# Performance work log

Measured on AMD Instinct MI355X. Metric: run time of the kernel, lower is better.

Reference implementation:

```python
import jax, jax.numpy as jnp
import numpy as np

PERIODS = [4, 2, 1]   # base_periods[:n_period]
TEMPERATURE = 0.1
TOPM = 20
EPS = 1e-12


def _l2norm(v, axis):
    n = jnp.sqrt(jnp.sum(v * v, axis=axis, keepdims=True))
    return v / jnp.maximum(n, EPS)


def decompose_mg(x):
    """x: [B, L, C] -> mg: [G, B, L, C] (offset removed, as in torch code)."""
    B, L, C = x.shape
    mg = []
    for g in PERIODS:
        cur = x.reshape(B, L // g, g, C).mean(axis=2)      # unfold(size=g, step=g).mean(-1)
        cur = jnp.repeat(cur, g, axis=1)                   # repeat_interleave back to L
        mg.append(cur)
    mg = jnp.stack(mg, axis=0)                             # [G, B, L, C]
    return mg - mg[:, :, -1:, :]                           # remove per-series last-step offset


def extract_channel_state(mg):
    """mg: [G, B, L, C] -> [G, B, C, 4] (mean, std, slope, mean |diff|)."""
    L = mg.shape[2]
    mean = mg.mean(axis=2)
    std = mg.std(axis=2)                                   # unbiased=False (ddof=0)
    slope = (mg[:, :, -1, :] - mg[:, :, 0, :]) / float(L - 1)
    abs_diff = jnp.abs(mg[:, :, 1:, :] - mg[:, :, :-1, :]).mean(axis=2)
    return jnp.stack([mean, std, slope, abs_diff], axis=-1)


def setup_inputs() -> dict:
    key = jax.random.key(0)
    k1, k2, k3 = jax.random.split(key, 3)
    B, L, C, G, T, P = 32, 512, 64, 3, 10000, 96
    x = jax.random.normal(k1, (B, L, C), dtype=jnp.float32)
    pool_state = jax.random.normal(k2, (G, T, C, 4), dtype=jnp.float32)
    y_pool = jax.random.normal(k3, (T, P, C), dtype=jnp.float32)
    return {"x": x, "pool_state": pool_state, "y_pool": y_pool}


def reference(x, pool_state, y_pool):
    # Multi-scale decomposition of query batch
    q_mg = decompose_mg(x)                                  # [G, B, L, C]
    q_state = extract_channel_state(q_mg)                   # [G, B, C, 4]
    # Normalized channel-state similarity vs candidate pool
    q = _l2norm(q_state, axis=-1)
    p = _l2norm(pool_state, axis=-1)
    sim = jnp.einsum('gbcd,gtcd->gbct', q, p)               # [G, B, C, T]
    sim = sim.mean(axis=0)                                  # combine granularities -> [B, C, T]
    # Top-m retrieval per (batch, channel)
    vals, idx = jax.lax.top_k(sim, TOPM)                    # [B, C, M]
    w = jax.nn.softmax(vals / TEMPERATURE, axis=-1)         # [B, C, M]
    # Gather retrieved future windows, channelwise: y_pool [T, P, C]
    C = y_pool.shape[2]
    y_ct = jnp.transpose(y_pool, (2, 0, 1))                 # [C, T, P]
    gathered = y_ct[jnp.arange(C)[None, :, None], idx]      # [B, C, M, P]
    out = jnp.einsum('bcm,bcmp->bpc', w, gathered)          # [B, P, C]
    return out
```

## Files before the change

kernel.cpp:

```cpp
#include <hip/hip_runtime.h>
#include <hip/hip_fp16.h>
#include <math.h>

#define NB 32
#define NL 512
#define NC 64
#define NG 3
#define NT 10000
#define NP 96
#define TOPM 20
#define M1 8
#define NCH 256
#define CHUNK 40
#define QK 16
#define NCAND 64
#define PNBLK 1250
#define P16STR ((size_t)NT * NC)

union H2U { uint2 u; __half2 h[2]; };

__global__ __launch_bounds__(512) void pre_kernel(const float* __restrict__ x,
                                                  const float* __restrict__ ps,
                                                  double* __restrict__ q,
                                                  uint2* __restrict__ phat16) {
  __shared__ double s_sum[8][3][64], s_sq[8][3][64], s_abs[8][3][64];
  __shared__ double s_first[3][64], s_last[3][64];
  if (blockIdx.x < NB) {
    const int b = blockIdx.x, w = threadIdx.x >> 6, c = threadIdx.x & 63;
    const float* xp = x + (size_t)b * NL * NC + c;
    const int l0 = w * 64;
    double sum[3] = {0, 0, 0}, sumsq[3] = {0, 0, 0}, sumabs[3] = {0, 0, 0};
    double prev[3] = {0, 0, 0}, first[3] = {0, 0, 0};
    if (w > 0) {
      double e0 = xp[(l0 - 4) * NC], e1 = xp[(l0 - 3) * NC];
      double e2 = xp[(l0 - 2) * NC], e3 = xp[(l0 - 1) * NC];
      prev[2] = e3; prev[1] = (e2 + e3) * 0.5; prev[0] = (e0 + e1 + e2 + e3) * 0.25;
    }
    double acc2 = 0.0, acc4 = 0.0;
    for (int i = 0; i < 64; ++i) {
      const int l = l0 + i;
      double v = (double)xp[l * NC];
      sum[2] += v; sumsq[2] += v * v;
      if (l == 0) first[2] = v; else sumabs[2] += fabs(v - prev[2]);
      prev[2] = v;
      acc2 += v;
      if (l & 1) {
        double cur = acc2 * 0.5; acc2 = 0.0;
        sum[1] += cur; sumsq[1] += cur * cur;
        if (l == 1) first[1] = cur; else sumabs[1] += fabs(cur - prev[1]);
        prev[1] = cur;
      }
      acc4 += v;
      if ((l & 3) == 3) {
        double cur = acc4 * 0.25; acc4 = 0.0;
        sum[0] += cur; sumsq[0] += cur * cur;
        if (l == 3) first[0] = cur; else sumabs[0] += fabs(cur - prev[0]);
        prev[0] = cur;
      }
    }
    for (int g = 0; g < 3; ++g) {
      s_sum[w][g][c] = sum[g]; s_sq[w][g][c] = sumsq[g]; s_abs[w][g][c] = sumabs[g];
    }
    if (w == 0) { for (int g = 0; g < 3; ++g) s_first[g][c] = first[g]; }
    if (w == 7) { for (int g = 0; g < 3; ++g) s_last[g][c] = prev[g]; }
    __syncthreads();
    if (w == 0) {
      const double J[3] = {128.0, 256.0, 512.0};
      for (int g = 0; g < 3; ++g) {
        double S = 0, Q2 = 0, A = 0;
        for (int ww = 0; ww < 8; ++ww) {
          S += s_sum[ww][g][c]; Q2 += s_sq[ww][g][c]; A += s_abs[ww][g][c];
        }
        double mean = S / J[g];
        double var = Q2 / J[g] - mean * mean; if (var < 0.0) var = 0.0;
        double last = s_last[g][c];
        double s0 = mean - last;
        double s1 = sqrt(var);
        double s2 = (last - s_first[g][c]) * (1.0 / 511.0);
        double s3 = A * (1.0 / 511.0);
        double n = sqrt(s0 * s0 + s1 * s1 + s2 * s2 + s3 * s3);
        double inv = 1.0 / fmax(n, 1e-12);
        double* qp = q + ((((size_t)g * NB) + b) * NC + c) * 4;
        qp[0] = s0 * inv; qp[1] = s1 * inv; qp[2] = s2 * inv; qp[3] = s3 * inv;
      }
    }
  } else {
    const int i = (blockIdx.x - NB) * 512 + threadIdx.x;
    if (i < NT * NC) {
#pragma unroll
      for (int g = 0; g < 3; ++g) {
        const size_t off = ((size_t)g * NT * NC + i) * 4;
        const float4 pv = *reinterpret_cast<const float4*>(ps + off);
        double p0 = pv.x, p1 = pv.y, p2 = pv.z, p3 = pv.w;
        double inv = 1.0 / fmax(sqrt(p0 * p0 + p1 * p1 + p2 * p2 + p3 * p3), 1e-12);
        H2U o;
        o.h[0] = __halves2half2(__float2half_rn((float)(p0 * inv)),
                                __float2half_rn((float)(p1 * inv)));
        o.h[1] = __halves2half2(__float2half_rn((float)(p2 * inv)),
                                __float2half_rn((float)(p3 * inv)));
        phat16[(size_t)g * P16STR + i] = o.u;
      }
    }
  }
}

__device__ __forceinline__ void insert8(float s, int ti, float val[M1], int idx[M1]) {
  float cv = s; int ci = ti;
#pragma unroll
  for (int m = 0; m < M1; ++m) {
    bool sw = cv > val[m];
    float tv = sw ? val[m] : cv; int tx = sw ? idx[m] : ci;
    val[m] = sw ? cv : val[m];   idx[m] = sw ? ci : idx[m];
    cv = tv; ci = tx;
  }
}

#if defined(__has_builtin)
#if __has_builtin(__builtin_amdgcn_fdot2)
#define HAVE_FDOT2 1
#endif
#endif

__device__ __forceinline__ float sim_dot(const uint2* __restrict__ p16,
                                         size_t o,
#ifdef HAVE_FDOT2
                                         const __half2 qh[6]
#else
                                         const float qv[12]
#endif
                                         ) {
  H2U a0, a1, a2;
  a0.u = p16[o];
  a1.u = p16[P16STR + o];
  a2.u = p16[2 * P16STR + o];
#ifdef HAVE_FDOT2
  float s = 0.f;
  s = __builtin_amdgcn_fdot2(qh[0], a0.h[0], s, false);
  s = __builtin_amdgcn_fdot2(qh[1], a0.h[1], s, false);
  s = __builtin_amdgcn_fdot2(qh[2], a1.h[0], s, false);
  s = __builtin_amdgcn_fdot2(qh[3], a1.h[1], s, false);
  s = __builtin_amdgcn_fdot2(qh[4], a2.h[0], s, false);
  s = __builtin_amdgcn_fdot2(qh[5], a2.h[1], s, false);
  return s;
#else
  float2 f0 = __half22float2(a0.h[0]), f1 = __half22float2(a0.h[1]);
  float2 f2 = __half22float2(a1.h[0]), f3 = __half22float2(a1.h[1]);
  float2 f4 = __half22float2(a2.h[0]), f5 = __half22float2(a2.h[1]);
  return qv[0] * f0.x + qv[1] * f0.y + qv[2] * f1.x + qv[3] * f1.y +
         qv[4] * f2.x + qv[5] * f2.y + qv[6] * f3.x + qv[7] * f3.y +
         qv[8] * f4.x + qv[9] * f4.y + qv[10] * f5.x + qv[11] * f5.y;
#endif
}

__global__ __launch_bounds__(1024, 8) void sim32_kernel(
    const uint2* __restrict__ p16, const double* __restrict__ q,
    float* __restrict__ cval, int* __restrict__ cidx) {
  const int wav = threadIdx.x >> 6;
  const int c = threadIdx.x & 63;
  const int b = blockIdx.x * 16 + wav;
  const int ch = blockIdx.y;
#ifdef HAVE_FDOT2
  __half2 qh[6];
#pragma unroll
  for (int g = 0; g < 3; ++g) {
    const double* qp = q + ((((size_t)g * NB) + b) * NC + c) * 4;
    qh[g * 2 + 0] = __halves2half2(__float2half_rn((float)(qp[0] * (1.0 / 3.0))),
                                   __float2half_rn((float)(qp[1] * (1.0 / 3.0))));
    qh[g * 2 + 1] = __halves2half2(__float2half_rn((float)(qp[2] * (1.0 / 3.0))),
                                   __float2half_rn((float)(qp[3] * (1.0 / 3.0))));
  }
#else
  float qv[12];
#pragma unroll
  for (int g = 0; g < 3; ++g) {
    const double* qp = q + ((((size_t)g * NB) + b) * NC + c) * 4;
#pragma unroll
    for (int j = 0; j < 4; ++j) qv[g * 4 + j] = (float)(qp[j] * (1.0 / 3.0));
  }
#endif
  float val[M1]; int idx[M1];
#pragma unroll
  for (int m = 0; m < M1; ++m) { val[m] = -1e30f; idx[m] = 0; }
  int t0 = ch * CHUNK;
  int t1 = t0 + CHUNK; if (t1 > NT) t1 = NT;
  for (int t = t0; t + 1 < t1; t += 2) {
    const size_t oA = (size_t)t * NC + c;
    const size_t oB = oA + NC;
#ifdef HAVE_FDOT2
    float sA = sim_dot(p16, oA, qh);
    float sB = sim_dot(p16, oB, qh);
#else
    float sA = sim_dot(p16, oA, qv);
    float sB = sim_dot(p16, oB, qv);
#endif
    if (sA > val[M1 - 1]) insert8(sA, t, val, idx);
    if (sB > val[M1 - 1]) insert8(sB, t + 1, val, idx);
  }
  float* vo = cval + ((((size_t)b * NC) + c) * NCH + ch) * M1;
  int* io = cidx + ((((size_t)b * NC) + c) * NCH + ch) * M1;
#pragma unroll
  for (int m = 0; m < M1; ++m) { vo[m] = val[m]; io[m] = idx[m]; }
}

__device__ __forceinline__ unsigned long long mk_key(float v, int t) {
  unsigned u = __float_as_uint(v);
  u = (u & 0x80000000u) ? ~u : (u | 0x80000000u);
  return ((unsigned long long)u << 32) | (unsigned long long)(0xFFFFFFFFu - (unsigned)t);
}

__global__ __launch_bounds__(128) void merge_gather_kernel(
    const float* __restrict__ cval, const int* __restrict__ cidx,
    const float* __restrict__ ps, const double* __restrict__ q,
    const float* __restrict__ y, float* __restrict__ out) {
  const int c = blockIdx.x, b = blockIdx.y;
  __shared__ float v_s[NCH * M1];
  __shared__ int i_s[NCH * M1];
  __shared__ int ct_s[NCAND];
  __shared__ double rv_s[NCAND];
  __shared__ double m0_s, inv_s;
  __shared__ double e_s[TOPM];
  __shared__ int ts_s[TOPM];
  __shared__ float w2_s[TOPM];
  __shared__ int t2_s[TOPM];
  const int n = NCH * M1;
  const size_t row = (size_t)b * NC + c;
  const float4* vin = reinterpret_cast<const float4*>(cval + row * n);
  const int4* iin = reinterpret_cast<const int4*>(cidx + row * n);
  for (int k = threadIdx.x; k < n / 4; k += 128) {
    *reinterpret_cast<float4*>(&v_s[k * 4]) = vin[k];
    *reinterpret_cast<int4*>(&i_s[k * 4]) = iin[k];
  }
  __syncthreads();
  {
    const int w = threadIdx.x >> 6, lane = threadIdx.x & 63;
    const int lane32 = lane & 31;
    const int qtr = (w << 1) | (lane >> 5);
    const int l0 = (qtr * 64 + lane32 * 2) * M1;
    const int l1 = l0 + M1;
    int p0 = 0, p1 = 0;
    unsigned long long k0 = mk_key(v_s[l0], i_s[l0]);
    unsigned long long k1 = mk_key(v_s[l1], i_s[l1]);
    for (int r = 0; r < QK; ++r) {
      unsigned long long me = k0 > k1 ? k0 : k1;
      unsigned long long km = me;
#pragma unroll
      for (int st = 1; st < 32; st <<= 1) {
        unsigned long long k2 = __shfl_xor(km, st);
        km = k2 > km ? k2 : km;
      }
      if (lane32 == r)
        ct_s[qtr * QK + r] = (int)(0xFFFFFFFFu - (unsigned)(km & 0xFFFFFFFFull));
      if (me == km) {
        if (k0 >= k1) {
          ++p0; k0 = (p0 < M1) ? mk_key(v_s[l0 + p0], i_s[l0 + p0]) : 0ull;
        } else {
          ++p1; k1 = (p1 < M1) ? mk_key(v_s[l1 + p1], i_s[l1 + p1]) : 0ull;
        }
      }
    }
  }
  __syncthreads();
  double myv = -1e300; int myt = 0x7fffffff;
  if (threadIdx.x < NCAND) {
    myt = ct_s[threadIdx.x];
    double s = 0.0;
#pragma unroll
    for (int g = 0; g < 3; ++g) {
      const double* qp = q + ((((size_t)g * NB) + b) * NC + c) * 4;
      const float4 pv = *reinterpret_cast<const float4*>(
          ps + ((((size_t)g * NT) + myt) * NC + c) * 4);
      double pp0 = pv.x, pp1 = pv.y, pp2 = pv.z, pp3 = pv.w;
      double ss = pp0 * pp0 + pp1 * pp1 + pp2 * pp2 + pp3 * pp3;
      double dot = qp[0] * pp0 + qp[1] * pp1 + qp[2] * pp2 + qp[3] * pp3;
      s += dot / fmax(sqrt(ss), 1e-12);
    }
    myv = s * (1.0 / 3.0);
    rv_s[threadIdx.x] = myv;
  }
  __syncthreads();
  int rank = -1;
  if (threadIdx.x < NCAND) {
    rank = 0;
    for (int j = 0; j < NCAND; ++j) {
      double vj = rv_s[j]; int tj = ct_s[j];
      rank += (vj > myv) || (vj == myv && tj < myt);
    }
    if (rank == 0) m0_s = myv;
  }
  __syncthreads();
  if (rank >= 0 && rank < TOPM) { e_s[rank] = exp((myv - m0_s) * 10.0); ts_s[rank] = myt; }
  __syncthreads();
  if (threadIdx.x == 0) {
    double sum = 0.0;
#pragma unroll
    for (int m = 0; m < TOPM; ++m) sum += e_s[m];
    inv_s = 1.0 / sum;
  }
  __syncthreads();
  if (threadIdx.x < TOPM) {
    const int t = ts_s[threadIdx.x];
    int pos = 0;
#pragma unroll
    for (int j = 0; j < TOPM; ++j) pos += (ts_s[j] < t);
    w2_s[pos] = (float)(e_s[threadIdx.x] * inv_s);
    t2_s[pos] = t;
  }
  __syncthreads();
  const int p = threadIdx.x;
  if (p < NP) {
    float acc = 0.f;
#pragma unroll
    for (int m = 0; m < TOPM; ++m)
      acc += w2_s[m] * y[(((size_t)t2_s[m]) * NP + p) * NC + c];
    out[(((size_t)b * NP) + p) * NC + c] = acc;
  }
}

__global__ __launch_bounds__(256) void sim_topk_inline_kernel(
    const float* __restrict__ ps, const double* __restrict__ q,
    double* __restrict__ cval, int* __restrict__ cidx, int nch, int chunk) {
  const int wav = threadIdx.x >> 6;
  const int c = threadIdx.x & 63;
  const int b = blockIdx.y * 4 + wav;
  const int ch = blockIdx.x;
  double qv[3][4];
#pragma unroll
  for (int g = 0; g < 3; ++g) {
    const double* qp = q + ((((size_t)g * NB) + b) * NC + c) * 4;
    qv[g][0] = qp[0]; qv[g][1] = qp[1]; qv[g][2] = qp[2]; qv[g][3] = qp[3];
  }
  double val[TOPM]; int idx[TOPM];
#pragma unroll
  for (int m = 0; m < TOPM; ++m) { val[m] = -1e300; idx[m] = 0; }
  int t0 = ch * chunk;
  int t1 = t0 + chunk; if (t1 > NT) t1 = NT;
  for (int t = t0; t < t1; ++t) {
    double s = 0.0;
#pragma unroll
    for (int g = 0; g < 3; ++g) {
      const float4 pv = *reinterpret_cast<const float4*>(
          ps + ((((size_t)g * NT) + t) * NC + c) * 4);
      double p0 = pv.x, p1 = pv.y, p2 = pv.z, p3 = pv.w;
      double ss = p0 * p0 + p1 * p1 + p2 * p2 + p3 * p3;
      double dot = qv[g][0] * p0 + qv[g][1] * p1 + qv[g][2] * p2 + qv[g][3] * p3;
      s += dot / fmax(sqrt(ss), 1e-12);
    }
    s *= (1.0 / 3.0);
    if (s > val[TOPM - 1]) {
      double cv = s; int ci = t;
#pragma unroll
      for (int m = 0; m < TOPM; ++m) {
        bool sw = cv > val[m];
        double tv = sw ? val[m] : cv; int ti = sw ? idx[m] : ci;
        val[m] = sw ? cv : val[m];    idx[m] = sw ? ci : idx[m];
        cv = tv; ci = ti;
      }
    }
  }
  double* vout = cval + ((((size_t)b * NC) + c) * nch + ch) * TOPM;
  int* iout = cidx + ((((size_t)b * NC) + c) * nch + ch) * TOPM;
#pragma unroll
  for (int m = 0; m < TOPM; ++m) { vout[m] = val[m]; iout[m] = idx[m]; }
}

__global__ __launch_bounds__(128) void merge_gather_old_kernel(
    const double* __restrict__ cval, const int* __restrict__ cidx,
    const float* __restrict__ y, float* __restrict__ out, int nch) {
  const int c = blockIdx.x;
  const int b = blockIdx.y;
  __shared__ float w_s[TOPM];
  __shared__ int i_s[TOPM];
  if (threadIdx.x == 0) {
    double val[TOPM]; int idx[TOPM];
#pragma unroll
    for (int m = 0; m < TOPM; ++m) { val[m] = -1e300; idx[m] = 0; }
    const double* vin = cval + (((size_t)b * NC) + c) * nch * TOPM;
    const int* iin = cidx + (((size_t)b * NC) + c) * nch * TOPM;
    for (int k = 0; k < nch; ++k) {
      const int base = k * TOPM;
      for (int m = 0; m < TOPM; ++m) {
        double s = vin[base + m];
        if (!(s > val[TOPM - 1])) break;
        double cv = s; int ci = iin[base + m];
#pragma unroll
        for (int mm = 0; mm < TOPM; ++mm) {
          bool sw = cv > val[mm];
          double tv = sw ? val[mm] : cv; int ti = sw ? idx[mm] : ci;
          val[mm] = sw ? cv : val[mm];   idx[mm] = sw ? ci : idx[mm];
          cv = tv; ci = ti;
        }
      }
    }
    double mx = val[0];
    double e[TOPM]; double sum = 0.0;
#pragma unroll
    for (int m = 0; m < TOPM; ++m) { e[m] = exp((val[m] - mx) * 10.0); sum += e[m]; }
    double inv = 1.0 / sum;
#pragma unroll
    for (int m = 0; m < TOPM; ++m) { w_s[m] = (float)(e[m] * inv); i_s[m] = idx[m]; }
  }
  __syncthreads();
  const int p = threadIdx.x;
  if (p < NP) {
    float acc = 0.f;
#pragma unroll
    for (int m = 0; m < TOPM; ++m)
      acc += w_s[m] * y[(((size_t)i_s[m]) * NP + p) * NC + c];
    out[(((size_t)b * NP) + p) * NC + c] = acc;
  }
}

extern "C" void kernel_launch(void* const* d_in, const int* in_sizes, int n_in,
                              void* d_out, int out_size, void* d_ws, size_t ws_size,
                              hipStream_t stream) {
  const float* x = (const float*)d_in[0];
  const float* ps = (const float*)d_in[1];
  const float* y = (const float*)d_in[2];
  float* out = (float*)d_out;
  char* ws = (char*)d_ws;

  const size_t qbytes = (size_t)NG * NB * NC * 4 * sizeof(double);
  const size_t phat16bytes = (size_t)NG * NT * NC * 8;
  const size_t cvalbytes = (size_t)NB * NC * NCH * M1 * sizeof(float);
  const size_t cidxbytes = cvalbytes;

  double* qbuf = (double*)ws;

  if (ws_size >= qbytes + phat16bytes + cvalbytes + cidxbytes) {
    uint2* phat16 = (uint2*)(ws + qbytes);
    float* cval = (float*)(ws + qbytes + phat16bytes);
    int* cidx = (int*)((char*)cval + cvalbytes);
    pre_kernel<<<dim3(NB + PNBLK), dim3(512), 0, stream>>>(x, ps, qbuf, phat16);
    sim32_kernel<<<dim3(NB / 16, NCH), dim3(1024), 0, stream>>>(phat16, qbuf,
                                                                cval, cidx);
    merge_gather_kernel<<<dim3(NC, NB), dim3(128), 0, stream>>>(cval, cidx, ps,
                                                                qbuf, y, out);
  } else {
    pre_kernel<<<dim3(NB), dim3(512), 0, stream>>>(x, ps, qbuf, (uint2*)nullptr);
    const size_t per_ch = (size_t)NB * NC * TOPM * (sizeof(double) + sizeof(int));
    int nch = 1;
    if (ws_size > qbytes) {
      size_t mc = (ws_size - qbytes) / per_ch;
      nch = mc < 32 ? (int)mc : 32;
      if (nch < 1) nch = 1;
    }
    const int chunk = (NT + nch - 1) / nch;
    double* fcval = (double*)(ws + qbytes);
    int* fcidx = (int*)((char*)fcval + (size_t)NB * NC * nch * TOPM * sizeof(double));
    sim_topk_inline_kernel<<<dim3(nch, NB / 4), dim3(256), 0, stream>>>(
        ps, qbuf, fcval, fcidx, nch, chunk);
    merge_gather_old_kernel<<<dim3(NC, NB), dim3(128), 0, stream>>>(fcval, fcidx, y,
                                                                    out, nch);
  }
}
```

Measured before the change: 144.2 us.

## Pack top-k candidates into 32-bit keys and bucket the y gather by time index

Candidates in the similarity pass are now stored as 32-bit keys: a half-precision score with a 16-bit time index. This halves candidate storage and replaces 64-bit merge keys with 32-bit ones. The final weighted gather is split into three kernels. The merge kernel writes softmax weights and bins each selection by time index with atomics. A per-time-index kernel then loads whole y rows through LDS and writes weighted partials, and a final kernel sums the partials. This trades the strided per-channel reads of y for coalesced row reads, but adds atomics, a large partial buffer, two extra launches, and a fixed bin capacity of 64 that silently drops entries beyond it.

```diff
diff --git a/kernel.cpp b/kernel.cpp
--- a/kernel.cpp
+++ b/kernel.cpp
@@ -15,6 +15,8 @@
 #define QK 16
 #define NCAND 64
 #define PNBLK 1250
+#define NENT (NB * NC * TOPM)
+#define BINCAP 64
 #define P16STR ((size_t)NT * NC)
 
 union H2U { uint2 u; __half2 h[2]; };
@@ -104,14 +106,20 @@
   }
 }
 
-__device__ __forceinline__ void insert8(float s, int ti, float val[M1], int idx[M1]) {
-  float cv = s; int ci = ti;
+__device__ __forceinline__ unsigned mkkey16(float v, int t) {
+  unsigned h = (unsigned)__half_as_ushort(__float2half_rn(v));
+  h = (h & 0x8000u) ? ((~h) & 0xFFFFu) : (h | 0x8000u);
+  return (h << 16) | (0xFFFFu - (unsigned)t);
+}
+
+__device__ __forceinline__ void insert8k(unsigned k, unsigned key[M1]) {
+  unsigned cv = k;
 #pragma unroll
   for (int m = 0; m < M1; ++m) {
-    bool sw = cv > val[m];
-    float tv = sw ? val[m] : cv; int tx = sw ? idx[m] : ci;
-    val[m] = sw ? cv : val[m];   idx[m] = sw ? ci : idx[m];
-    cv = tv; ci = tx;
+    bool sw = cv > key[m];
+    unsigned tv = sw ? key[m] : cv;
+    key[m] = sw ? cv : key[m];
+    cv = tv;
   }
 }
 
@@ -154,7 +162,11 @@
 
 __global__ __launch_bounds__(1024, 8) void sim32_kernel(
     const uint2* __restrict__ p16, const double* __restrict__ q,
-    float* __restrict__ cval, int* __restrict__ cidx) {
+    unsigned* __restrict__ ckey, int* __restrict__ hist) {
+  if (blockIdx.x == 0 && blockIdx.y < 10) {
+    const int idx = blockIdx.y * 1024 + threadIdx.x;
+    if (idx < NT) hist[idx] = 0;
+  }
   const int wav = threadIdx.x >> 6;
   const int c = threadIdx.x & 63;
   const int b = blockIdx.x * 16 + wav;
@@ -178,58 +190,47 @@
     for (int j = 0; j < 4; ++j) qv[g * 4 + j] = (float)(qp[j] * (1.0 / 3.0));
   }
 #endif
-  float val[M1]; int idx[M1];
-#pragma unroll
-  for (int m = 0; m < M1; ++m) { val[m] = -1e30f; idx[m] = 0; }
+  unsigned key[M1];
+#pragma unroll
+  for (int m = 0; m < M1; ++m) key[m] = 0u;
   int t0 = ch * CHUNK;
   int t1 = t0 + CHUNK; if (t1 > NT) t1 = NT;
   for (int t = t0; t + 1 < t1; t += 2) {
     const size_t oA = (size_t)t * NC + c;
     const size_t oB = oA + NC;
 #ifdef HAVE_FDOT2
-    float sA = sim_dot(p16, oA, qh);
-    float sB = sim_dot(p16, oB, qh);
+    const float sA = sim_dot(p16, oA, qh);
+    const float sB = sim_dot(p16, oB, qh);
 #else
-    float sA = sim_dot(p16, oA, qv);
-    float sB = sim_dot(p16, oB, qv);
+    const float sA = sim_dot(p16, oA, qv);
+    const float sB = sim_dot(p16, oB, qv);
 #endif
-    if (sA > val[M1 - 1]) insert8(sA, t, val, idx);
-    if (sB > val[M1 - 1]) insert8(sB, t + 1, val, idx);
-  }
-  float* vo = cval + ((((size_t)b * NC) + c) * NCH + ch) * M1;
-  int* io = cidx + ((((size_t)b * NC) + c) * NCH + ch) * M1;
-#pragma unroll
-  for (int m = 0; m < M1; ++m) { vo[m] = val[m]; io[m] = idx[m]; }
-}
-
-__device__ __forceinline__ unsigned long long mk_key(float v, int t) {
-  unsigned u = __float_as_uint(v);
-  u = (u & 0x80000000u) ? ~u : (u | 0x80000000u);
-  return ((unsigned long long)u << 32) | (unsigned long long)(0xFFFFFFFFu - (unsigned)t);
-}
-
-__global__ __launch_bounds__(128) void merge_gather_kernel(
-    const float* __restrict__ cval, const int* __restrict__ cidx,
-    const float* __restrict__ ps, const double* __restrict__ q,
-    const float* __restrict__ y, float* __restrict__ out) {
+    const unsigned kA = mkkey16(sA, t);
+    const unsigned kB = mkkey16(sB, t + 1);
+    if (kA > key[M1 - 1]) insert8k(kA, key);
+    if (kB > key[M1 - 1]) insert8k(kB, key);
+  }
+  unsigned* ko = ckey + ((((size_t)b * NC) + c) * NCH + ch) * M1;
+  *reinterpret_cast<uint4*>(ko) = make_uint4(key[0], key[1], key[2], key[3]);
+  *reinterpret_cast<uint4*>(ko + 4) = make_uint4(key[4], key[5], key[6], key[7]);
+}
+
+__global__ __launch_bounds__(128) void merge_rerank_kernel(
+    const unsigned* __restrict__ ckey, const float* __restrict__ ps,
+    const double* __restrict__ q, float* __restrict__ w_out,
+    int* __restrict__ t_out, int* __restrict__ hist, int* __restrict__ bin_slot) {
   const int c = blockIdx.x, b = blockIdx.y;
-  __shared__ float v_s[NCH * M1];
-  __shared__ int i_s[NCH * M1];
+  __shared__ unsigned k_s[NCH * M1];
   __shared__ int ct_s[NCAND];
   __shared__ double rv_s[NCAND];
   __shared__ double m0_s, inv_s;
   __shared__ double e_s[TOPM];
   __shared__ int ts_s[TOPM];
-  __shared__ float w2_s[TOPM];
-  __shared__ int t2_s[TOPM];
   const int n = NCH * M1;
   const size_t row = (size_t)b * NC + c;
-  const float4* vin = reinterpret_cast<const float4*>(cval + row * n);
-  const int4* iin = reinterpret_cast<const int4*>(cidx + row * n);
-  for (int k = threadIdx.x; k < n / 4; k += 128) {
-    *reinterpret_cast<float4*>(&v_s[k * 4]) = vin[k];
-    *reinterpret_cast<int4*>(&i_s[k * 4]) = iin[k];
-  }
+  const uint4* kin = reinterpret_cast<const uint4*>(ckey + row * n);
+  for (int k = threadIdx.x; k < n / 4; k += 128)
+    *reinterpret_cast<uint4*>(&k_s[k * 4]) = kin[k];
   __syncthreads();
   {
     const int w = threadIdx.x >> 6, lane = threadIdx.x & 63;
@@ -238,24 +239,19 @@
     const int l0 = (qtr * 64 + lane32 * 2) * M1;
     const int l1 = l0 + M1;
     int p0 = 0, p1 = 0;
-    unsigned long long k0 = mk_key(v_s[l0], i_s[l0]);
-    unsigned long long k1 = mk_key(v_s[l1], i_s[l1]);
+    unsigned k0 = k_s[l0], k1 = k_s[l1];
     for (int r = 0; r < QK; ++r) {
-      unsigned long long me = k0 > k1 ? k0 : k1;
-      unsigned long long km = me;
+      const unsigned me = k0 > k1 ? k0 : k1;
+      unsigned km = me;
 #pragma unroll
       for (int st = 1; st < 32; st <<= 1) {
-        unsigned long long k2 = __shfl_xor(km, st);
+        const unsigned k2 = __shfl_xor(km, st);
         km = k2 > km ? k2 : km;
       }
-      if (lane32 == r)
-        ct_s[qtr * QK + r] = (int)(0xFFFFFFFFu - (unsigned)(km & 0xFFFFFFFFull));
+      if (lane32 == r) ct_s[qtr * QK + r] = (int)(0xFFFFu - (km & 0xFFFFu));
       if (me == km) {
-        if (k0 >= k1) {
-          ++p0; k0 = (p0 < M1) ? mk_key(v_s[l0 + p0], i_s[l0 + p0]) : 0ull;
-        } else {
-          ++p1; k1 = (p1 < M1) ? mk_key(v_s[l1 + p1], i_s[l1 + p1]) : 0ull;
-        }
+        if (k0 >= k1) { ++p0; k0 = (p0 < M1) ? k_s[l0 + p0] : 0u; }
+        else          { ++p1; k1 = (p1 < M1) ? k_s[l1 + p1] : 0u; }
       }
     }
   }
@@ -299,21 +295,62 @@
   __syncthreads();
   if (threadIdx.x < TOPM) {
     const int t = ts_s[threadIdx.x];
-    int pos = 0;
-#pragma unroll
-    for (int j = 0; j < TOPM; ++j) pos += (ts_s[j] < t);
-    w2_s[pos] = (float)(e_s[threadIdx.x] * inv_s);
-    t2_s[pos] = t;
-  }
-  __syncthreads();
+    const int i = (int)(row * TOPM) + threadIdx.x;
+    w_out[i] = (float)(e_s[threadIdx.x] * inv_s);
+    t_out[i] = t;
+    const int pos = atomicAdd(&hist[t], 1);
+    if (pos < BINCAP) bin_slot[t * BINCAP + pos] = i;
+  }
+}
+
+__global__ __launch_bounds__(256) void process_kernel(
+    const float* __restrict__ y, const int* __restrict__ hist,
+    const int* __restrict__ bin_slot, const float* __restrict__ w_out,
+    float* __restrict__ partial) {
+  const int t = blockIdx.x;
+  int k = hist[t];
+  if (k == 0) return;
+  if (k > BINCAP) k = BINCAP;
+  __shared__ float lds[NP * 65];
+  __shared__ float w_l[BINCAP];
+  __shared__ int i_l[BINCAP];
+  __shared__ int c_l[BINCAP];
+  const float4* yrow = reinterpret_cast<const float4*>(y + (size_t)t * NP * NC);
+#pragma unroll
+  for (int r = 0; r < 6; ++r) {
+    const int e4 = threadIdx.x + r * 256;
+    const float4 v = yrow[e4];
+    const int p = e4 >> 4;
+    const int c = (e4 & 15) * 4;
+    lds[p * 65 + c] = v.x; lds[p * 65 + c + 1] = v.y;
+    lds[p * 65 + c + 2] = v.z; lds[p * 65 + c + 3] = v.w;
+  }
+  if (threadIdx.x < k) {
+    const int i = bin_slot[t * BINCAP + threadIdx.x];
+    i_l[threadIdx.x] = i;
+    w_l[threadIdx.x] = w_out[i];
+    c_l[threadIdx.x] = (i / TOPM) & 63;
+  }
+  __syncthreads();
+  const int h = threadIdx.x >> 7;
+  const int p = threadIdx.x & 127;
+  for (int e = h; e < k; e += 2) {
+    if (p < NP)
+      partial[(size_t)i_l[e] * NP + p] = w_l[e] * lds[p * 65 + c_l[e]];
+  }
+}
+
+__global__ __launch_bounds__(128) void final_kernel(const float* __restrict__ partial,
+                                                    float* __restrict__ out) {
+  const int row = blockIdx.x;
   const int p = threadIdx.x;
-  if (p < NP) {
-    float acc = 0.f;
-#pragma unroll
-    for (int m = 0; m < TOPM; ++m)
-      acc += w2_s[m] * y[(((size_t)t2_s[m]) * NP + p) * NC + c];
-    out[(((size_t)b * NP) + p) * NC + c] = acc;
-  }
+  if (p >= NP) return;
+  const int b = row >> 6, c = row & 63;
+  const float* pp = partial + (size_t)row * TOPM * NP + p;
+  float acc = 0.f;
+#pragma unroll
+  for (int m = 0; m < TOPM; ++m) acc += pp[m * NP];
+  out[(((size_t)b * NP) + p) * NC + c] = acc;
 }
 
 __global__ __launch_bounds__(256) void sim_topk_inline_kernel(
@@ -421,20 +458,32 @@
 
   const size_t qbytes = (size_t)NG * NB * NC * 4 * sizeof(double);
   const size_t phat16bytes = (size_t)NG * NT * NC * 8;
-  const size_t cvalbytes = (size_t)NB * NC * NCH * M1 * sizeof(float);
-  const size_t cidxbytes = cvalbytes;
+  const size_t ckeybytes = (size_t)NB * NC * NCH * M1 * 4;
+  const size_t wtbytes = (size_t)NENT * 4;
+  const size_t histbytes = (size_t)NT * 4;
+  const size_t slotbytes = (size_t)NT * BINCAP * 4;
+  const size_t partbytes = (size_t)NENT * NP * 4;
 
   double* qbuf = (double*)ws;
-
-  if (ws_size >= qbytes + phat16bytes + cvalbytes + cidxbytes) {
-    uint2* phat16 = (uint2*)(ws + qbytes);
-    float* cval = (float*)(ws + qbytes + phat16bytes);
-    int* cidx = (int*)((char*)cval + cvalbytes);
+  size_t off = qbytes;
+  uint2* phat16 = (uint2*)(ws + off); off += phat16bytes;
+  unsigned* ckey = (unsigned*)(ws + off); off += ckeybytes;
+  float* w_out = (float*)(ws + off); off += wtbytes;
+  int* t_out = (int*)(ws + off); off += wtbytes;
+  int* hist = (int*)(ws + off); off += histbytes;
+  off = (off + 7) & ~(size_t)7;
+  int* bin_slot = (int*)(ws + off); off += slotbytes;
+  float* partial = (float*)(ws + off); off += partbytes;
+
+  if (ws_size >= off) {
     pre_kernel<<<dim3(NB + PNBLK), dim3(512), 0, stream>>>(x, ps, qbuf, phat16);
     sim32_kernel<<<dim3(NB / 16, NCH), dim3(1024), 0, stream>>>(phat16, qbuf,
-                                                                cval, cidx);
-    merge_gather_kernel<<<dim3(NC, NB), dim3(128), 0, stream>>>(cval, cidx, ps,
-                                                                qbuf, y, out);
+                                                                ckey, hist);
+    merge_rerank_kernel<<<dim3(NC, NB), dim3(128), 0, stream>>>(
+        ckey, ps, qbuf, w_out, t_out, hist, bin_slot);
+    process_kernel<<<dim3(NT), dim3(256), 0, stream>>>(y, hist, bin_slot,
+                                                       w_out, partial);
+    final_kernel<<<dim3(NB * NC), dim3(128), 0, stream>>>(partial, out);
   } else {
     pre_kernel<<<dim3(NB), dim3(512), 0, stream>>>(x, ps, qbuf, (uint2*)nullptr);
     const size_t per_ch = (size_t)NB * NC * TOPM * (sizeof(double) + sizeof(int));
```

Result: faster. 117.2 us (-18.7%).
